# Performance work log

Measured on AMD Instinct MI355X. Metric: run time of the kernel, lower is better.

## Reference

```python
import jax, jax.numpy as jnp
import numpy as np

N_NODES = 100000
N_EDGES = 1600000
D = 64


def setup_inputs() -> dict:
    key = jax.random.key(0)
    k1, k2, k3, k4 = jax.random.split(key, 4)
    x = jax.random.normal(k1, (N_NODES, D), dtype=jnp.float32)
    # glorot-uniform scale for Linear weight [out_dim, in_dim]
    stdv = np.sqrt(6.0 / (D + D)).astype(np.float32)
    W = jax.random.uniform(k2, (D, D), dtype=jnp.float32, minval=-stdv, maxval=stdv)
    bias = jnp.zeros((D,), dtype=jnp.float32)  # forward() uses a zero bias
    edge_index = jax.random.randint(k3, (2, N_EDGES), 0, N_NODES, dtype=jnp.int64)
    counts = jax.random.randint(k4, (N_NODES,), 0, 16, dtype=jnp.int64)
    out_edge_index = jnp.arange(N_EDGES, dtype=jnp.int64)
    return {"x": x, "W": W, "bias": bias, "edge_index": edge_index,
            "counts": counts, "out_edge_index": out_edge_index, "layer_i": 0}


def reference(x, W, bias, edge_index, counts, out_edge_index, layer_i):
    # GCN layer: y = x @ W^T; gather by source; scatter-sum by destination; add bias.
    # counts / out_edge_index / layer_i are layout hints for the fused CUDA kernel
    # (mygraph.gcn) and do not change the math.
    y = x @ W.T                              # [N, D_out]
    src = edge_index[0]                      # [E]
    dst = edge_index[1]                      # [E]
    msgs = y[src]                            # [E, D_out] edge gather
    out = jax.ops.segment_sum(msgs, dst, num_segments=x.shape[0])  # [N, D_out]
    return out + bias
```

## Files before the change

### kernel.cpp

```cpp
#include <hip/hip_runtime.h>


#define DIM 64
#define BN 64
#define BN_SHIFT 6
#define BN_MASK 63
#define NB_MAX 2048
#define PB 256
#define KMAX 8
#define CAPE 1536
#define OVF_MAX 262144

__device__ __forceinline__ unsigned short f32_to_bf16_rne(float f) {
    unsigned u = __float_as_uint(f);
    unsigned r = u + 0x7FFFu + ((u >> 16) & 1u);
    return (unsigned short)(r >> 16);
}

__global__ __launch_bounds__(1024) void fused_prep_reg_kernel(
        const float* __restrict__ x, const int* __restrict__ ei,
        ushort4* __restrict__ xb4, int* __restrict__ gcnt,
        int* __restrict__ binned, int* __restrict__ ovf,
        int* __restrict__ ovfcnt, int E, int N, int nb, int total4) {
    __shared__ int h[NB_MAX];
    const int t = threadIdx.x;
    const int bid = blockIdx.x;

    for (int b = t; b < nb; b += 1024) h[b] = 0;
    __syncthreads();

    int es[KMAX], ds[KMAX];
    #pragma unroll
    for (int k = 0; k < KMAX; ++k) {
        int e = (k * PB + bid) * 1024 + t;
        if (e < E) {
            es[k] = ei[e];
            ds[k] = ei[E + e];
            atomicAdd(&h[ds[k] >> BN_SHIFT], 1);
        } else {
            ds[k] = -1;
        }
    }

    for (int i = bid * 1024 + t; i < total4; i += PB * 1024) {
        float4 v = ((const float4*)x)[i];
        ushort4 o;
        o.x = f32_to_bf16_rne(v.x); o.y = f32_to_bf16_rne(v.y);
        o.z = f32_to_bf16_rne(v.z); o.w = f32_to_bf16_rne(v.w);
        xb4[i] = o;
    }
    if (bid == 0 && t < 16) {
        ushort4 z; z.x = 0; z.y = 0; z.z = 0; z.w = 0;
        xb4[(size_t)N * 16 + t] = z;
    }
    __syncthreads();

    for (int b = t; b < nb; b += 1024) {
        int c = h[b];
        int base = (c > 0) ? atomicAdd(&gcnt[b], c) : 0;
        h[b] = b * CAPE + base;
    }
    __syncthreads();

    #pragma unroll
    for (int k = 0; k < KMAX; ++k) {
        if (ds[k] >= 0) {
            int b = ds[k] >> BN_SHIFT;
            int p = atomicAdd(&h[b], 1);
            if (p < b * CAPE + CAPE) {
                binned[p] = (es[k] << BN_SHIFT) | (ds[k] & BN_MASK);
            } else {
                int q = atomicAdd(ovfcnt, 1);
                if (q < OVF_MAX) { ovf[2 * q] = es[k]; ovf[2 * q + 1] = ds[k]; }
            }
        }
    }
}

__global__ __launch_bounds__(1024) void fused_prep_kernel(
        const float* __restrict__ x, const int* __restrict__ ei,
        ushort4* __restrict__ xb4, int* __restrict__ gcnt,
        int* __restrict__ binned, int* __restrict__ ovf,
        int* __restrict__ ovfcnt, int E, int N, int nb, int total4) {
    __shared__ int h[NB_MAX];
    const int t = threadIdx.x;
    const int bid = blockIdx.x;

    for (int b = t; b < nb; b += 1024) h[b] = 0;
    __syncthreads();

    for (int i = bid * 1024 + t; i < total4; i += PB * 1024) {
        float4 v = ((const float4*)x)[i];
        ushort4 o;
        o.x = f32_to_bf16_rne(v.x); o.y = f32_to_bf16_rne(v.y);
        o.z = f32_to_bf16_rne(v.z); o.w = f32_to_bf16_rne(v.w);
        xb4[i] = o;
    }
    if (bid == 0 && t < 16) {
        ushort4 z; z.x = 0; z.y = 0; z.z = 0; z.w = 0;
        xb4[(size_t)N * 16 + t] = z;
    }

    for (int e = bid * 1024 + t; e < E; e += PB * 1024)
        atomicAdd(&h[ei[E + e] >> BN_SHIFT], 1);
    __syncthreads();

    for (int b = t; b < nb; b += 1024) {
        int c = h[b];
        int base = (c > 0) ? atomicAdd(&gcnt[b], c) : 0;
        h[b] = b * CAPE + base;
    }
    __syncthreads();

    for (int e = bid * 1024 + t; e < E; e += PB * 1024) {
        int s = ei[e];
        int d = ei[E + e];
        int b = d >> BN_SHIFT;
        int p = atomicAdd(&h[b], 1);
        if (p < b * CAPE + CAPE) {
            binned[p] = (s << BN_SHIFT) | (d & BN_MASK);
        } else {
            int q = atomicAdd(ovfcnt, 1);
            if (q < OVF_MAX) { ovf[2 * q] = s; ovf[2 * q + 1] = d; }
        }
    }
}

__device__ __forceinline__ void acc8(float (&a)[8], const uint4& v) {
    a[0] += __uint_as_float(v.x << 16); a[1] += __uint_as_float(v.x & 0xFFFF0000u);
    a[2] += __uint_as_float(v.y << 16); a[3] += __uint_as_float(v.y & 0xFFFF0000u);
    a[4] += __uint_as_float(v.z << 16); a[5] += __uint_as_float(v.z & 0xFFFF0000u);
    a[6] += __uint_as_float(v.w << 16); a[7] += __uint_as_float(v.w & 0xFFFF0000u);
}

__device__ __forceinline__ float epilogue64(const float (&a)[8],
                                            const float (&wv)[DIM], float bb) {
    float r0 = bb, r1 = 0.f, r2 = 0.f, r3 = 0.f;
    #pragma unroll
    for (int k = 0; k < DIM; k += 4) {
        r0 += __int_as_float(__builtin_amdgcn_readlane(
                  __float_as_int(a[(k + 0) & 7]), (k + 0) >> 3)) * wv[k + 0];
        r1 += __int_as_float(__builtin_amdgcn_readlane(
                  __float_as_int(a[(k + 1) & 7]), (k + 1) >> 3)) * wv[k + 1];
        r2 += __int_as_float(__builtin_amdgcn_readlane(
                  __float_as_int(a[(k + 2) & 7]), (k + 2) >> 3)) * wv[k + 2];
        r3 += __int_as_float(__builtin_amdgcn_readlane(
                  __float_as_int(a[(k + 3) & 7]), (k + 3) >> 3)) * wv[k + 3];
    }
    return (r0 + r1) + (r2 + r3);
}

__global__ __launch_bounds__(256) void sort_gather_kernel(
        const unsigned short* __restrict__ xh, const float* __restrict__ xf,
        const int* __restrict__ binned, const int* __restrict__ gcnt,
        const int* __restrict__ ovf, const int* __restrict__ ovfcnt,
        const float* __restrict__ W, const float* __restrict__ bias,
        float* __restrict__ out, int N) {
    __shared__ int cnt[BN];
    __shared__ int basel[BN + 1];
    __shared__ int tmp[BN];
    __shared__ int slds[CAPE];

    const int t = threadIdx.x;
    const int g = blockIdx.x;
    const int lane = t & 63;
    const int wid = t >> 6;
    const int node0 = g << BN_SHIFT;

    float wv[DIM];
    #pragma unroll
    for (int k4 = 0; k4 < DIM / 4; ++k4) {
        float4 tw = *(const float4*)(W + (size_t)lane * DIM + k4 * 4);
        wv[k4 * 4 + 0] = tw.x; wv[k4 * 4 + 1] = tw.y;
        wv[k4 * 4 + 2] = tw.z; wv[k4 * 4 + 3] = tw.w;
    }
    const float bb = bias[lane];

    const int seg0 = g * CAPE;
    int len = gcnt[g];
    if (len > CAPE) len = CAPE;
    const int seg1 = seg0 + len;

    if (t < BN) cnt[t] = 0;
    __syncthreads();

    for (int i = seg0 + t; i < seg1; i += 256)
        atomicAdd(&cnt[binned[i] & BN_MASK], 1);
    __syncthreads();

    int myv = (t < BN) ? cnt[t] : 0;
    if (t < BN) tmp[t] = myv;
    __syncthreads();
    #pragma unroll
    for (int d = 1; d < BN; d <<= 1) {
        int u = (t < BN && t >= d) ? tmp[t - d] : 0;
        __syncthreads();
        if (t < BN) tmp[t] += u;
        __syncthreads();
    }
    if (t < BN) basel[t] = tmp[t] - myv;
    if (t == BN - 1) basel[BN] = tmp[t];
    if (t < BN) cnt[t] = tmp[t] - myv;
    __syncthreads();

    for (int i = seg0 + t; i < seg1; i += 256) {
        int v = binned[i];
        int p = atomicAdd(&cnt[v & BN_MASK], 1);
        slds[p] = v >> BN_SHIFT;
    }
    __syncthreads();

    const int sub8 = lane >> 3;
    const int fb   = (lane & 7) << 3;
    const int zrow = N;
    for (int q = wid; q < (BN >> 2); q += 4) {
        const int nl = q << 2;
        int b0 = basel[nl + 0], e0 = basel[nl + 1];
        int b1 = basel[nl + 1], e1 = basel[nl + 2];
        int b2 = basel[nl + 2], e2 = basel[nl + 3];
        int b3 = basel[nl + 3], e3 = basel[nl + 4];
        int c0 = (e0 - b0 + 7) >> 3, c1 = (e1 - b1 + 7) >> 3;
        int c2 = (e2 - b2 + 7) >> 3, c3 = (e3 - b3 + 7) >> 3;
        int cmax = max(max(c0, c1), max(c2, c3));
        cmax = __builtin_amdgcn_readfirstlane(cmax);

        float A0[8] = {0.f,0.f,0.f,0.f,0.f,0.f,0.f,0.f};
        float A1[8] = {0.f,0.f,0.f,0.f,0.f,0.f,0.f,0.f};
        float A2[8] = {0.f,0.f,0.f,0.f,0.f,0.f,0.f,0.f};
        float A3[8] = {0.f,0.f,0.f,0.f,0.f,0.f,0.f,0.f};

        for (int c = 0; c < cmax; ++c) {
            const int o = (c << 3) + sub8;
            int i0 = b0 + o, i1 = b1 + o, i2 = b2 + o, i3 = b3 + o;
            int s0 = slds[min(i0, CAPE - 1)];
            int s1 = slds[min(i1, CAPE - 1)];
            int s2 = slds[min(i2, CAPE - 1)];
            int s3 = slds[min(i3, CAPE - 1)];
            s0 = (i0 < e0) ? s0 : zrow;
            s1 = (i1 < e1) ? s1 : zrow;
            s2 = (i2 < e2) ? s2 : zrow;
            s3 = (i3 < e3) ? s3 : zrow;
            uint4 v0 = *(const uint4*)(xh + (size_t)s0 * DIM + fb);
            uint4 v1 = *(const uint4*)(xh + (size_t)s1 * DIM + fb);
            uint4 v2 = *(const uint4*)(xh + (size_t)s2 * DIM + fb);
            uint4 v3 = *(const uint4*)(xh + (size_t)s3 * DIM + fb);
            acc8(A0, v0); acc8(A1, v1); acc8(A2, v2); acc8(A3, v3);
        }

        #pragma unroll
        for (int d = 8; d <= 32; d <<= 1) {
            #pragma unroll
            for (int j = 0; j < 8; ++j) {
                A0[j] += __shfl_xor(A0[j], d, 64);
                A1[j] += __shfl_xor(A1[j], d, 64);
                A2[j] += __shfl_xor(A2[j], d, 64);
                A3[j] += __shfl_xor(A3[j], d, 64);
            }
        }

        const int n0 = node0 + nl;
        if (n0 + 0 < N) out[(size_t)(n0 + 0) * DIM + lane] = epilogue64(A0, wv, bb);
        if (n0 + 1 < N) out[(size_t)(n0 + 1) * DIM + lane] = epilogue64(A1, wv, bb);
        if (n0 + 2 < N) out[(size_t)(n0 + 2) * DIM + lane] = epilogue64(A2, wv, bb);
        if (n0 + 3 < N) out[(size_t)(n0 + 3) * DIM + lane] = epilogue64(A3, wv, bb);
    }

    __syncthreads();
    int oc = *ovfcnt;
    if (oc > 0) {
        if (oc > OVF_MAX) oc = OVF_MAX;
        for (int i = wid; i < oc; i += 4) {
            int s = ovf[2 * i];
            int d = ovf[2 * i + 1];
            if ((d >> BN_SHIFT) == g) {
                float v = xf[(size_t)s * DIM + lane];
                float r = epilogue64(*(const float(*)[8])&v, wv, 0.f);
                float rr0 = 0.f, rr1 = 0.f, rr2 = 0.f, rr3 = 0.f;
                #pragma unroll
                for (int k = 0; k < DIM; k += 4) {
                    rr0 += __int_as_float(__builtin_amdgcn_readlane(__float_as_int(v), k + 0)) * wv[k + 0];
                    rr1 += __int_as_float(__builtin_amdgcn_readlane(__float_as_int(v), k + 1)) * wv[k + 1];
                    rr2 += __int_as_float(__builtin_amdgcn_readlane(__float_as_int(v), k + 2)) * wv[k + 2];
                    rr3 += __int_as_float(__builtin_amdgcn_readlane(__float_as_int(v), k + 3)) * wv[k + 3];
                }
                (void)r;
                atomicAdd(&out[(size_t)d * DIM + lane], (rr0 + rr1) + (rr2 + rr3));
            }
        }
    }
}

__global__ void gcn_scatter_kernel(const float* __restrict__ x,
                                   const int* __restrict__ edge_index,
                                   float* __restrict__ out, int n_edges) {
    int gid = blockIdx.x * blockDim.x + threadIdx.x;
    int e = gid >> 4;
    if (e >= n_edges) return;
    int j = (gid & 15) << 2;
    int src = edge_index[e];
    int dst = edge_index[n_edges + e];
    const float4 v = *(const float4*)(x + (size_t)src * DIM + j);
    float* o = out + (size_t)dst * DIM + j;
    atomicAdd(o + 0, v.x); atomicAdd(o + 1, v.y);
    atomicAdd(o + 2, v.z); atomicAdd(o + 3, v.w);
}

__global__ void gcn_linear_inplace_kernel(float* __restrict__ out,
                                          const float* __restrict__ W,
                                          const float* __restrict__ bias,
                                          int n_nodes) {
    __shared__ float Wt[DIM * DIM];
    __shared__ float rows[4][DIM];
    int tid = threadIdx.x;
    int col = tid & 63;
    int r = tid >> 6;
    for (int i = tid; i < DIM * DIM; i += 256) {
        int c = i >> 6, k = i & 63;
        Wt[k * DIM + c] = W[i];
    }
    int row = blockIdx.x * 4 + r;
    if (row < n_nodes) rows[r][col] = out[(size_t)row * DIM + col];
    __syncthreads();
    if (row < n_nodes) {
        float a = 0.f;
        #pragma unroll
        for (int k = 0; k < DIM; ++k) a += rows[r][k] * Wt[k * DIM + col];
        out[(size_t)row * DIM + col] = a + bias[col];
    }
}

extern "C" void kernel_launch(void* const* d_in, const int* in_sizes, int n_in,
                              void* d_out, int out_size, void* d_ws, size_t ws_size,
                              hipStream_t stream) {
    const float* x          = (const float*)d_in[0];
    const float* W          = (const float*)d_in[1];
    const float* bias       = (const float*)d_in[2];
    const int*   edge_index = (const int*)d_in[3];

    const int E = in_sizes[3] / 2;
    const int N = in_sizes[0] / DIM;
    float* out = (float*)d_out;

    const int nb = (N + BN - 1) >> BN_SHIFT;

    auto align256 = [](size_t v) { return (v + 255) & ~(size_t)255; };
    const size_t xb_b   = align256(((size_t)N + 1) * DIM * 2);
    const size_t bin_b  = align256((size_t)nb * CAPE * 4);
    const size_t cnt_b  = align256(((size_t)nb + 64) * 4);
    const size_t ovf_b  = align256((size_t)OVF_MAX * 2 * 4);
    const size_t needA = xb_b + bin_b + cnt_b + ovf_b;

    if (nb <= NB_MAX && N < (1 << 24) && ws_size >= needA) {
        char* p = (char*)d_ws;
        ushort4* xb4 = (ushort4*)p;          p += xb_b;
        int* binned  = (int*)p;              p += bin_b;
        int* gcnt    = (int*)p;              p += cnt_b;
        int* ovf     = (int*)p;
        int* ovfcnt  = gcnt + nb;

        const int total4 = N * DIM / 4;

        hipMemsetAsync(gcnt, 0, cnt_b, stream);
        if ((long long)E <= (long long)PB * 1024 * KMAX) {
            fused_prep_reg_kernel<<<PB, 1024, 0, stream>>>(
                x, edge_index, xb4, gcnt, binned, ovf, ovfcnt, E, N, nb, total4);
        } else {
            fused_prep_kernel<<<PB, 1024, 0, stream>>>(
                x, edge_index, xb4, gcnt, binned, ovf, ovfcnt, E, N, nb, total4);
        }
        sort_gather_kernel<<<nb, 256, 0, stream>>>(
            (const unsigned short*)xb4, x, binned, gcnt, ovf, ovfcnt,
            W, bias, out, N);
    } else {
        hipMemsetAsync(d_out, 0, (size_t)out_size * sizeof(float), stream);
        long long total = (long long)E * 16;
        int grid = (int)((total + 255) / 256);
        gcn_scatter_kernel<<<grid, 256, 0, stream>>>(x, edge_index, out, E);
        int lgrid = (N + 3) / 4;
        gcn_linear_inplace_kernel<<<lgrid, 256, 0, stream>>>(out, W, bias, N);
    }
}
```

Baseline: 195.8 us.

## Replace per-node readlane epilogue with split-bf16 MFMA matmul over staged aggregates

Aggregated node sums are now packed into high and low bf16 halves and staged in shared memory. After a block barrier, each wave runs a 16x64 tile matmul against W with three MFMA 16x16x32 products per k-half (hi*hi, lo*hi, hi*lo) to keep near-fp32 accuracy. This replaces the scalar readlane-based 64-term dot product per output and removes the 64-register W preload, which may also ease register pressure. The cost is extra shared memory, an additional barrier, bf16 packing work, and per-block conversion of W.

```diff
diff --git a/kernel.cpp b/kernel.cpp
--- a/kernel.cpp
+++ b/kernel.cpp
@@ -10,11 +10,31 @@
 #define KMAX 8
 #define CAPE 1536
 #define OVF_MAX 262144
+#define AGS 72
+
+typedef __attribute__((ext_vector_type(8))) short short8;
+typedef __attribute__((ext_vector_type(4))) float f32x4;
 
 __device__ __forceinline__ unsigned short f32_to_bf16_rne(float f) {
     unsigned u = __float_as_uint(f);
     unsigned r = u + 0x7FFFu + ((u >> 16) & 1u);
     return (unsigned short)(r >> 16);
+}
+
+__device__ __forceinline__ void pk2(float a, float b, unsigned &ph, unsigned &pl) {
+    unsigned ha = f32_to_bf16_rne(a);
+    unsigned hb = f32_to_bf16_rne(b);
+    ph = ha | (hb << 16);
+    float fa = __uint_as_float(ha << 16);
+    float fb = __uint_as_float(hb << 16);
+    unsigned la = f32_to_bf16_rne(a - fa);
+    unsigned lb = f32_to_bf16_rne(b - fb);
+    pl = la | (lb << 16);
+}
+
+__device__ __forceinline__ f32x4 mfma16(uint4 a, uint4 b, f32x4 c) {
+    return __builtin_amdgcn_mfma_f32_16x16x32_bf16(
+        __builtin_bit_cast(short8, a), __builtin_bit_cast(short8, b), c, 0, 0, 0);
 }
 
 __global__ __launch_bounds__(1024) void fused_prep_reg_kernel(
@@ -133,22 +153,20 @@
     a[6] += __uint_as_float(v.w << 16); a[7] += __uint_as_float(v.w & 0xFFFF0000u);
 }
 
-__device__ __forceinline__ float epilogue64(const float (&a)[8],
-                                            const float (&wv)[DIM], float bb) {
-    float r0 = bb, r1 = 0.f, r2 = 0.f, r3 = 0.f;
-    #pragma unroll
-    for (int k = 0; k < DIM; k += 4) {
-        r0 += __int_as_float(__builtin_amdgcn_readlane(
-                  __float_as_int(a[(k + 0) & 7]), (k + 0) >> 3)) * wv[k + 0];
-        r1 += __int_as_float(__builtin_amdgcn_readlane(
-                  __float_as_int(a[(k + 1) & 7]), (k + 1) >> 3)) * wv[k + 1];
-        r2 += __int_as_float(__builtin_amdgcn_readlane(
-                  __float_as_int(a[(k + 2) & 7]), (k + 2) >> 3)) * wv[k + 2];
-        r3 += __int_as_float(__builtin_amdgcn_readlane(
-                  __float_as_int(a[(k + 3) & 7]), (k + 3) >> 3)) * wv[k + 3];
-    }
-    return (r0 + r1) + (r2 + r3);
-}
+#define PACK_STORE(AR, ROW)                                                   \
+    do {                                                                      \
+        unsigned ph0, ph1, ph2, ph3, pl0, pl1, pl2, pl3;                      \
+        pk2(AR[0], AR[1], ph0, pl0); pk2(AR[2], AR[3], ph1, pl1);             \
+        pk2(AR[4], AR[5], ph2, pl2); pk2(AR[6], AR[7], ph3, pl3);             \
+        const int dco = (lane & 7) << 3;                                      \
+        if (lane < 8) {                                                       \
+            uint4 v; v.x = ph0; v.y = ph1; v.z = ph2; v.w = ph3;              \
+            *(uint4*)&aggh[(ROW) * AGS + dco] = v;                            \
+        } else if (lane < 16) {                                               \
+            uint4 v; v.x = pl0; v.y = pl1; v.z = pl2; v.w = pl3;              \
+            *(uint4*)&aggl[(ROW) * AGS + dco] = v;                            \
+        }                                                                     \
+    } while (0)
 
 __global__ __launch_bounds__(256) void sort_gather_kernel(
         const unsigned short* __restrict__ xh, const float* __restrict__ xf,
@@ -160,21 +178,14 @@
     __shared__ int basel[BN + 1];
     __shared__ int tmp[BN];
     __shared__ int slds[CAPE];
+    __shared__ __align__(16) unsigned short aggh[BN * AGS];
+    __shared__ __align__(16) unsigned short aggl[BN * AGS];
 
     const int t = threadIdx.x;
     const int g = blockIdx.x;
     const int lane = t & 63;
     const int wid = t >> 6;
     const int node0 = g << BN_SHIFT;
-
-    float wv[DIM];
-    #pragma unroll
-    for (int k4 = 0; k4 < DIM / 4; ++k4) {
-        float4 tw = *(const float4*)(W + (size_t)lane * DIM + k4 * 4);
-        wv[k4 * 4 + 0] = tw.x; wv[k4 * 4 + 1] = tw.y;
-        wv[k4 * 4 + 2] = tw.z; wv[k4 * 4 + 3] = tw.w;
-    }
-    const float bb = bias[lane];
 
     const int seg0 = g * CAPE;
     int len = gcnt[g];
@@ -258,11 +269,62 @@
             }
         }
 
-        const int n0 = node0 + nl;
-        if (n0 + 0 < N) out[(size_t)(n0 + 0) * DIM + lane] = epilogue64(A0, wv, bb);
-        if (n0 + 1 < N) out[(size_t)(n0 + 1) * DIM + lane] = epilogue64(A1, wv, bb);
-        if (n0 + 2 < N) out[(size_t)(n0 + 2) * DIM + lane] = epilogue64(A2, wv, bb);
-        if (n0 + 3 < N) out[(size_t)(n0 + 3) * DIM + lane] = epilogue64(A3, wv, bb);
+        PACK_STORE(A0, nl + 0);
+        PACK_STORE(A1, nl + 1);
+        PACK_STORE(A2, nl + 2);
+        PACK_STORE(A3, nl + 3);
+    }
+
+    __syncthreads();
+
+    {
+        const int mbase = wid << 4;
+        const int l15 = lane & 15;
+        const int kq  = lane >> 4;
+
+        const unsigned short* arow_h = aggh + (mbase + l15) * AGS + (kq << 3);
+        const unsigned short* arow_l = aggl + (mbase + l15) * AGS + (kq << 3);
+        uint4 ah0 = *(const uint4*)(arow_h);
+        uint4 ah1 = *(const uint4*)(arow_h + 32);
+        uint4 al0 = *(const uint4*)(arow_l);
+        uint4 al1 = *(const uint4*)(arow_l + 32);
+
+        f32x4 acc[4];
+        #pragma unroll
+        for (int n = 0; n < 4; ++n) {
+            float bb = bias[(n << 4) + l15];
+            acc[n] = (f32x4){bb, bb, bb, bb};
+        }
+
+        #pragma unroll
+        for (int n = 0; n < 4; ++n) {
+            const float* wr = W + (size_t)((n << 4) + l15) * DIM + (kq << 3);
+            float4 wa = *(const float4*)(wr);
+            float4 wb = *(const float4*)(wr + 4);
+            float4 wc = *(const float4*)(wr + 32);
+            float4 wd = *(const float4*)(wr + 36);
+            uint4 bh0, bl0, bh1, bl1;
+            pk2(wa.x, wa.y, bh0.x, bl0.x); pk2(wa.z, wa.w, bh0.y, bl0.y);
+            pk2(wb.x, wb.y, bh0.z, bl0.z); pk2(wb.z, wb.w, bh0.w, bl0.w);
+            pk2(wc.x, wc.y, bh1.x, bl1.x); pk2(wc.z, wc.w, bh1.y, bl1.y);
+            pk2(wd.x, wd.y, bh1.z, bl1.z); pk2(wd.z, wd.w, bh1.w, bl1.w);
+            acc[n] = mfma16(ah0, bh0, acc[n]);
+            acc[n] = mfma16(al0, bh0, acc[n]);
+            acc[n] = mfma16(ah0, bl0, acc[n]);
+            acc[n] = mfma16(ah1, bh1, acc[n]);
+            acc[n] = mfma16(al1, bh1, acc[n]);
+            acc[n] = mfma16(ah1, bl1, acc[n]);
+        }
+
+        #pragma unroll
+        for (int n = 0; n < 4; ++n) {
+            #pragma unroll
+            for (int i = 0; i < 4; ++i) {
+                int node = node0 + mbase + (kq << 2) + i;
+                if (node < N)
+                    out[(size_t)node * DIM + (n << 4) + l15] = acc[n][i];
+            }
+        }
     }
 
     __syncthreads();
@@ -274,16 +336,14 @@
             int d = ovf[2 * i + 1];
             if ((d >> BN_SHIFT) == g) {
                 float v = xf[(size_t)s * DIM + lane];
-                float r = epilogue64(*(const float(*)[8])&v, wv, 0.f);
                 float rr0 = 0.f, rr1 = 0.f, rr2 = 0.f, rr3 = 0.f;
                 #pragma unroll
                 for (int k = 0; k < DIM; k += 4) {
-                    rr0 += __int_as_float(__builtin_amdgcn_readlane(__float_as_int(v), k + 0)) * wv[k + 0];
-                    rr1 += __int_as_float(__builtin_amdgcn_readlane(__float_as_int(v), k + 1)) * wv[k + 1];
-                    rr2 += __int_as_float(__builtin_amdgcn_readlane(__float_as_int(v), k + 2)) * wv[k + 2];
-                    rr3 += __int_as_float(__builtin_amdgcn_readlane(__float_as_int(v), k + 3)) * wv[k + 3];
+                    rr0 += __int_as_float(__builtin_amdgcn_readlane(__float_as_int(v), k + 0)) * W[(size_t)lane * DIM + k + 0];
+                    rr1 += __int_as_float(__builtin_amdgcn_readlane(__float_as_int(v), k + 1)) * W[(size_t)lane * DIM + k + 1];
+                    rr2 += __int_as_float(__builtin_amdgcn_readlane(__float_as_int(v), k + 2)) * W[(size_t)lane * DIM + k + 2];
+                    rr3 += __int_as_float(__builtin_amdgcn_readlane(__float_as_int(v), k + 3)) * W[(size_t)lane * DIM + k + 3];
                 }
-                (void)r;
                 atomicAdd(&out[(size_t)d * DIM + lane], (rr0 + rr1) + (rr2 + rr3));
             }
         }
```

New measurement: 175.6 us. -10.3%, faster.
